# Performance work log

Measured on AMD Instinct MI355X. Metric: run time of the kernel, lower is better.

## Reference

```python
import jax, jax.numpy as jnp
import numpy as np

VOCAB = 33
D = 256
B = 64
L = 4096


def setup_inputs() -> dict:
    key = jax.random.key(0)
    ks = jax.random.split(key, 7)
    X = jax.random.randint(ks[0], (B, L), 0, VOCAB, dtype=jnp.int64)
    valid_lens = jax.random.randint(ks[1], (B,), 0, L, dtype=jnp.int64)
    emb = jax.random.normal(ks[2], (VOCAB, D), dtype=jnp.float32)
    W1 = jax.random.normal(ks[3], (D, D), dtype=jnp.float32) * (1.0 / np.sqrt(D))
    b1 = jnp.zeros((D,), dtype=jnp.float32)
    W2 = jax.random.normal(ks[4], (D, D), dtype=jnp.float32) * (1.0 / np.sqrt(D))
    b2 = jnp.zeros((D,), dtype=jnp.float32)
    return {"X": X, "valid_lens": valid_lens, "emb": emb, "W1": W1, "b1": b1, "W2": W2, "b2": b2}


def reference(X, valid_lens, emb, W1, b1, W2, b2):
    # Embedding gather: [B, L, D]
    e = emb[X]
    # Length mask (on-device, no python loop): positions >= valid_len zeroed
    mask = (jnp.arange(L)[None, :] < valid_lens[:, None]).astype(e.dtype)  # [B, L]
    # Masked sum-pool over sequence -> [B, D]
    pooled = jnp.einsum("bld,bl->bd", e, mask)
    # Two-layer MLP with ReLU (dropout is identity in eval)
    h = jax.nn.relu(pooled @ W1 + b1)
    out = jax.nn.relu(h @ W2 + b2)
    return out
```

## Files before the change

kernel.cpp:

```cpp
#include <hip/hip_runtime.h>

#define B_SZ  64
#define L_SZ  4096
#define VOCAB 33
#define D_SZ  256
#define NT    512
#define NW    8
#define KS    2
#define KPG   128

__global__ __launch_bounds__(NT) void prot_net_fused(
    const int* __restrict__ X,
    const int* __restrict__ valid_lens,
    const float* __restrict__ emb,
    const float* __restrict__ W1,
    const float* __restrict__ b1,
    const float* __restrict__ W2,
    const float* __restrict__ b2,
    float* __restrict__ out)
{
    __shared__ int   s_cnt[NW][VOCAB];
    __shared__ float s_cntf[VOCAB];
    __shared__ float s_part[KS][D_SZ];
    __shared__ float s_vec[D_SZ];

    const int b   = blockIdx.x;
    const int tid = threadIdx.x;
    const int wv  = tid >> 6;
    const int g   = tid >> 8;
    const int d   = tid & (D_SZ - 1);

    float e[16];
    #pragma unroll
    for (int j = 0; j < 16; ++j)
        e[j] = emb[(g * 16 + j) * D_SZ + d];
    const float e16   = (g == 0) ? emb[32 * D_SZ + d] : 0.0f;
    const float bias1 = (tid < D_SZ) ? b1[tid] : 0.0f;
    const float bias2 = (tid < D_SZ) ? b2[tid] : 0.0f;
    const int   vl    = valid_lens[b];
    const int4* xrow4 = reinterpret_cast<const int4*>(X + (size_t)b * L_SZ);
    const int4  t0    = xrow4[tid];
    const int4  t1    = xrow4[tid + NT];

    for (int i = tid; i < NW * VOCAB; i += NT) ((int*)s_cnt)[i] = 0;
    __syncthreads();

    const int l0 = tid * 4;
    const int l1 = (tid + NT) * 4;
    if (l0 + 0 < vl) atomicAdd(&s_cnt[wv][t0.x], 1);
    if (l0 + 1 < vl) atomicAdd(&s_cnt[wv][t0.y], 1);
    if (l0 + 2 < vl) atomicAdd(&s_cnt[wv][t0.z], 1);
    if (l0 + 3 < vl) atomicAdd(&s_cnt[wv][t0.w], 1);
    if (l1 + 0 < vl) atomicAdd(&s_cnt[wv][t1.x], 1);
    if (l1 + 1 < vl) atomicAdd(&s_cnt[wv][t1.y], 1);
    if (l1 + 2 < vl) atomicAdd(&s_cnt[wv][t1.z], 1);
    if (l1 + 3 < vl) atomicAdd(&s_cnt[wv][t1.w], 1);
    __syncthreads();

    if (tid < VOCAB) {
        int c = 0;
        #pragma unroll
        for (int w = 0; w < NW; ++w) c += s_cnt[w][tid];
        s_cntf[tid] = (float)c;
    }
    __syncthreads();

    float p = 0.0f;
    #pragma unroll
    for (int j = 0; j < 16; ++j)
        p = fmaf(s_cntf[g * 16 + j], e[j], p);
    p = fmaf(s_cntf[32], e16, p);
    s_part[g][d] = p;
    __syncthreads();

    if (tid < D_SZ)
        s_vec[tid] = s_part[0][tid] + s_part[1][tid];
    __syncthreads();

    float acc = 0.0f;
    #pragma unroll
    for (int j = 0; j < KPG; ++j) {
        int k = g * KPG + j;
        acc = fmaf(s_vec[k], W1[k * D_SZ + d], acc);
    }
    s_part[g][d] = acc;
    __syncthreads();
    if (tid < D_SZ) {
        float h = bias1 + s_part[0][tid] + s_part[1][tid];
        s_vec[tid] = fmaxf(h, 0.0f);
    }
    __syncthreads();

    float acc2 = 0.0f;
    #pragma unroll
    for (int j = 0; j < KPG; ++j) {
        int k = g * KPG + j;
        acc2 = fmaf(s_vec[k], W2[k * D_SZ + d], acc2);
    }
    s_part[g][d] = acc2;
    __syncthreads();
    if (tid < D_SZ) {
        float o = bias2 + s_part[0][tid] + s_part[1][tid];
        out[(size_t)b * D_SZ + tid] = fmaxf(o, 0.0f);
    }
}

extern "C" void kernel_launch(void* const* d_in, const int* in_sizes, int n_in,
                              void* d_out, int out_size, void* d_ws, size_t ws_size,
                              hipStream_t stream) {
    const int*   X          = (const int*)d_in[0];
    const int*   valid_lens = (const int*)d_in[1];
    const float* emb        = (const float*)d_in[2];
    const float* W1         = (const float*)d_in[3];
    const float* b1         = (const float*)d_in[4];
    const float* W2         = (const float*)d_in[5];
    const float* b2         = (const float*)d_in[6];
    float* out = (float*)d_out;

    prot_net_fused<<<B_SZ, NT, 0, stream>>>(X, valid_lens, emb, W1, b1, W2, b2, out);
}
```

Measured before the change: 12.08 us.

## Vectorize columns as float4 and split K over eight groups per block

Each thread now owns four consecutive output columns loaded as float4, and the 512 threads split the reduction dimension into eight groups of 32 rows instead of two groups of 128. Each wave reduces its own slice of vocab counts directly, which removes one sync stage, and partial sums are combined in shared memory across the eight groups. The intent is shorter serial FMA chains with wider, fewer global loads of W1, W2 and emb. In exchange, the final cross-group reduction is larger and runs on only 64 threads.

```diff
diff --git a/kernel.cpp b/kernel.cpp
--- a/kernel.cpp
+++ b/kernel.cpp
@@ -6,8 +6,9 @@
 #define D_SZ  256
 #define NT    512
 #define NW    8
-#define KS    2
-#define KPG   128
+#define G     8
+#define KPG   32
+#define C     64
 
 __global__ __launch_bounds__(NT) void prot_net_fused(
     const int* __restrict__ X,
@@ -19,89 +20,145 @@
     const float* __restrict__ b2,
     float* __restrict__ out)
 {
-    __shared__ int   s_cnt[NW][VOCAB];
-    __shared__ float s_cntf[VOCAB];
-    __shared__ float s_part[KS][D_SZ];
-    __shared__ float s_vec[D_SZ];
+    __shared__ int    s_cnt[NW][VOCAB];
+    __shared__ float4 s_part[G][C];
+    __shared__ float  s_vec[D_SZ];
 
     const int b   = blockIdx.x;
     const int tid = threadIdx.x;
-    const int wv  = tid >> 6;
-    const int g   = tid >> 8;
-    const int d   = tid & (D_SZ - 1);
+    const int g   = tid >> 6;
+    const int c   = tid & 63;
 
-    float e[16];
+    const float4* emb4 = reinterpret_cast<const float4*>(emb);
+    const float4* W14  = reinterpret_cast<const float4*>(W1);
+    const float4* W24  = reinterpret_cast<const float4*>(W2);
+
+    float4 e4[4];
     #pragma unroll
-    for (int j = 0; j < 16; ++j)
-        e[j] = emb[(g * 16 + j) * D_SZ + d];
-    const float e16   = (g == 0) ? emb[32 * D_SZ + d] : 0.0f;
-    const float bias1 = (tid < D_SZ) ? b1[tid] : 0.0f;
-    const float bias2 = (tid < D_SZ) ? b2[tid] : 0.0f;
+    for (int j = 0; j < 4; ++j)
+        e4[j] = emb4[(g * 4 + j) * C + c];
+    float4 e32 = make_float4(0.f, 0.f, 0.f, 0.f);
+    if (g == 0) e32 = emb4[32 * C + c];
+
+    float4 bias1 = make_float4(0.f, 0.f, 0.f, 0.f);
+    float4 bias2 = make_float4(0.f, 0.f, 0.f, 0.f);
+    if (tid < C) {
+        bias1 = reinterpret_cast<const float4*>(b1)[tid];
+        bias2 = reinterpret_cast<const float4*>(b2)[tid];
+    }
     const int   vl    = valid_lens[b];
     const int4* xrow4 = reinterpret_cast<const int4*>(X + (size_t)b * L_SZ);
     const int4  t0    = xrow4[tid];
     const int4  t1    = xrow4[tid + NT];
 
-    for (int i = tid; i < NW * VOCAB; i += NT) ((int*)s_cnt)[i] = 0;
+    if (tid < NW * VOCAB) ((int*)s_cnt)[tid] = 0;
     __syncthreads();
 
     const int l0 = tid * 4;
     const int l1 = (tid + NT) * 4;
-    if (l0 + 0 < vl) atomicAdd(&s_cnt[wv][t0.x], 1);
-    if (l0 + 1 < vl) atomicAdd(&s_cnt[wv][t0.y], 1);
-    if (l0 + 2 < vl) atomicAdd(&s_cnt[wv][t0.z], 1);
-    if (l0 + 3 < vl) atomicAdd(&s_cnt[wv][t0.w], 1);
-    if (l1 + 0 < vl) atomicAdd(&s_cnt[wv][t1.x], 1);
-    if (l1 + 1 < vl) atomicAdd(&s_cnt[wv][t1.y], 1);
-    if (l1 + 2 < vl) atomicAdd(&s_cnt[wv][t1.z], 1);
-    if (l1 + 3 < vl) atomicAdd(&s_cnt[wv][t1.w], 1);
+    if (l0 + 0 < vl) atomicAdd(&s_cnt[g][t0.x], 1);
+    if (l0 + 1 < vl) atomicAdd(&s_cnt[g][t0.y], 1);
+    if (l0 + 2 < vl) atomicAdd(&s_cnt[g][t0.z], 1);
+    if (l0 + 3 < vl) atomicAdd(&s_cnt[g][t0.w], 1);
+    if (l1 + 0 < vl) atomicAdd(&s_cnt[g][t1.x], 1);
+    if (l1 + 1 < vl) atomicAdd(&s_cnt[g][t1.y], 1);
+    if (l1 + 2 < vl) atomicAdd(&s_cnt[g][t1.z], 1);
+    if (l1 + 3 < vl) atomicAdd(&s_cnt[g][t1.w], 1);
     __syncthreads();
 
-    if (tid < VOCAB) {
-        int c = 0;
+    float cf[4];
+    #pragma unroll
+    for (int j = 0; j < 4; ++j) {
+        int s = 0;
         #pragma unroll
-        for (int w = 0; w < NW; ++w) c += s_cnt[w][tid];
-        s_cntf[tid] = (float)c;
+        for (int w = 0; w < NW; ++w) s += s_cnt[w][g * 4 + j];
+        cf[j] = (float)s;
+    }
+    float c32 = 0.f;
+    if (g == 0) {
+        int s = 0;
+        #pragma unroll
+        for (int w = 0; w < NW; ++w) s += s_cnt[w][32];
+        c32 = (float)s;
+    }
+
+    float4 p = make_float4(0.f, 0.f, 0.f, 0.f);
+    #pragma unroll
+    for (int j = 0; j < 4; ++j) {
+        p.x = fmaf(cf[j], e4[j].x, p.x);
+        p.y = fmaf(cf[j], e4[j].y, p.y);
+        p.z = fmaf(cf[j], e4[j].z, p.z);
+        p.w = fmaf(cf[j], e4[j].w, p.w);
+    }
+    p.x = fmaf(c32, e32.x, p.x);
+    p.y = fmaf(c32, e32.y, p.y);
+    p.z = fmaf(c32, e32.z, p.z);
+    p.w = fmaf(c32, e32.w, p.w);
+    s_part[g][c] = p;
+    __syncthreads();
+
+    if (tid < C) {
+        float4 s = s_part[0][tid];
+        #pragma unroll
+        for (int g2 = 1; g2 < G; ++g2) {
+            float4 q = s_part[g2][tid];
+            s.x += q.x; s.y += q.y; s.z += q.z; s.w += q.w;
+        }
+        reinterpret_cast<float4*>(s_vec)[tid] = s;
     }
     __syncthreads();
 
-    float p = 0.0f;
-    #pragma unroll
-    for (int j = 0; j < 16; ++j)
-        p = fmaf(s_cntf[g * 16 + j], e[j], p);
-    p = fmaf(s_cntf[32], e16, p);
-    s_part[g][d] = p;
-    __syncthreads();
-
-    if (tid < D_SZ)
-        s_vec[tid] = s_part[0][tid] + s_part[1][tid];
-    __syncthreads();
-
-    float acc = 0.0f;
+    float4 acc = make_float4(0.f, 0.f, 0.f, 0.f);
     #pragma unroll
     for (int j = 0; j < KPG; ++j) {
         int k = g * KPG + j;
-        acc = fmaf(s_vec[k], W1[k * D_SZ + d], acc);
+        float  sv = s_vec[k];
+        float4 w  = W14[k * C + c];
+        acc.x = fmaf(sv, w.x, acc.x);
+        acc.y = fmaf(sv, w.y, acc.y);
+        acc.z = fmaf(sv, w.z, acc.z);
+        acc.w = fmaf(sv, w.w, acc.w);
     }
-    s_part[g][d] = acc;
+    s_part[g][c] = acc;
     __syncthreads();
-    if (tid < D_SZ) {
-        float h = bias1 + s_part[0][tid] + s_part[1][tid];
-        s_vec[tid] = fmaxf(h, 0.0f);
+
+    if (tid < C) {
+        float4 h = bias1;
+        #pragma unroll
+        for (int g2 = 0; g2 < G; ++g2) {
+            float4 q = s_part[g2][tid];
+            h.x += q.x; h.y += q.y; h.z += q.z; h.w += q.w;
+        }
+        h.x = fmaxf(h.x, 0.f); h.y = fmaxf(h.y, 0.f);
+        h.z = fmaxf(h.z, 0.f); h.w = fmaxf(h.w, 0.f);
+        reinterpret_cast<float4*>(s_vec)[tid] = h;
     }
     __syncthreads();
 
-    float acc2 = 0.0f;
+    float4 acc2 = make_float4(0.f, 0.f, 0.f, 0.f);
     #pragma unroll
     for (int j = 0; j < KPG; ++j) {
         int k = g * KPG + j;
-        acc2 = fmaf(s_vec[k], W2[k * D_SZ + d], acc2);
+        float  sv = s_vec[k];
+        float4 w  = W24[k * C + c];
+        acc2.x = fmaf(sv, w.x, acc2.x);
+        acc2.y = fmaf(sv, w.y, acc2.y);
+        acc2.z = fmaf(sv, w.z, acc2.z);
+        acc2.w = fmaf(sv, w.w, acc2.w);
     }
-    s_part[g][d] = acc2;
+    s_part[g][c] = acc2;
     __syncthreads();
-    if (tid < D_SZ) {
-        float o = bias2 + s_part[0][tid] + s_part[1][tid];
-        out[(size_t)b * D_SZ + tid] = fmaxf(o, 0.0f);
+
+    if (tid < C) {
+        float4 o = bias2;
+        #pragma unroll
+        for (int g2 = 0; g2 < G; ++g2) {
+            float4 q = s_part[g2][tid];
+            o.x += q.x; o.y += q.y; o.z += q.z; o.w += q.w;
+        }
+        o.x = fmaxf(o.x, 0.f); o.y = fmaxf(o.y, 0.f);
+        o.z = fmaxf(o.z, 0.f); o.w = fmaxf(o.w, 0.f);
+        reinterpret_cast<float4*>(out + (size_t)b * D_SZ)[tid] = o;
     }
 }
 
```

Result: faster. 11.47 us (-5.1%).
